# Kernel tuning notes

Hardware: AMD Instinct MI355X
Metric: run time of the kernel (lower is better)

## Reference

```python
import jax, jax.numpy as jnp
import numpy as np

VOCAB, EMBED, ENC_DIM, HIDDEN, ATTN = 32000, 512, 512, 1024, 128
SRC_LEN, TGT_LEN = 1024, 512


def setup_inputs() -> dict:
    key = jax.random.key(0)
    ks = jax.random.split(key, 16)
    s = lambda fan_in: 1.0 / np.sqrt(fan_in)
    inp = {
        "encoder_outputs": jax.random.normal(ks[0], (SRC_LEN, ENC_DIM), jnp.float32),
        "initial_h": jax.random.normal(ks[1], (HIDDEN,), jnp.float32),
        "initial_c": jnp.zeros((HIDDEN,), jnp.float32),
        "sos_token": 1,
        "target_seq": jax.random.randint(ks[2], (TGT_LEN,), 0, VOCAB, jnp.int32),
        # parameters
        "emb_table": jax.random.normal(ks[3], (VOCAB, EMBED), jnp.float32),
        "Wa_enc": jax.random.normal(ks[4], (ATTN, ENC_DIM), jnp.float32) * s(ENC_DIM),
        "Wa_h": jax.random.normal(ks[5], (ATTN, HIDDEN), jnp.float32) * s(HIDDEN),
        "v_a": jax.random.normal(ks[6], (ATTN,), jnp.float32) * s(ATTN),
        "W_ih": jax.random.normal(ks[7], (4 * HIDDEN, EMBED + ENC_DIM), jnp.float32) * s(EMBED + ENC_DIM),
        "W_hh": jax.random.normal(ks[8], (4 * HIDDEN, HIDDEN), jnp.float32) * s(HIDDEN),
        "b_ih": jnp.zeros((4 * HIDDEN,), jnp.float32),
        "b_hh": jnp.zeros((4 * HIDDEN,), jnp.float32),
        "W_out": jax.random.normal(ks[9], (VOCAB, HIDDEN), jnp.float32) * s(HIDDEN),
        "b_out": jnp.zeros((VOCAB,), jnp.float32),
    }
    return inp


def reference(encoder_outputs, initial_h, initial_c, sos_token, target_seq,
              emb_table, Wa_enc, Wa_h, v_a, W_ih, W_hh, b_ih, b_hh, W_out, b_out):
    # Teacher forcing with ratio 1.0: input token at step t is target_seq[t-1] (sos at t=0).
    prev_tokens = jnp.concatenate([jnp.array([sos_token], dtype=target_seq.dtype), target_seq[:-1]])
    embedded = emb_table[prev_tokens]                      # (T, E)
    enc_proj = encoder_outputs @ Wa_enc.T                  # (S, A), precomputed once

    def step(carry, emb_t):
        h, c = carry
        # Bahdanau attention: v^T tanh(W_enc e_s + W_h h)
        scores = jnp.tanh(enc_proj + Wa_h @ h) @ v_a       # (S,)
        attn = jax.nn.softmax(scores)                      # (S,)
        context = attn @ encoder_outputs                   # (ENC_DIM,)
        x = jnp.concatenate([emb_t, context])              # (E + ENC_DIM,)
        gates = W_ih @ x + b_ih + W_hh @ h + b_hh          # (4H,) order i,f,g,o
        i, f, g, o = jnp.split(gates, 4)
        c_new = jax.nn.sigmoid(f) * c + jax.nn.sigmoid(i) * jnp.tanh(g)
        h_new = jax.nn.sigmoid(o) * jnp.tanh(c_new)
        logits = W_out @ h_new + b_out                     # (V,)
        return (h_new, c_new), (logits, attn)

    (_, _), (all_logits, all_attn) = jax.lax.scan(step, (initial_h, initial_c), embedded)
    return all_logits, all_attn                            # (T, V), (T, S)
```

## Files before the change

### kernel.cpp

```cpp
#include <hip/hip_runtime.h>
#include <hip/hip_bf16.h>

#define VOCAB 32000
#define EMBED 512
#define ENCD  512
#define HID   1024
#define ATTN  128
#define SRC   1024
#define TGT   512
#define NB    64
#define NT    512
#define CHUNK 16

typedef __hip_bfloat16 bf16;
typedef _Float16 f16;
typedef __attribute__((ext_vector_type(2))) _Float16 f16x2;
typedef __attribute__((ext_vector_type(8))) _Float16 f16x8;
typedef __attribute__((ext_vector_type(8))) short bf16x8v;
typedef __attribute__((ext_vector_type(4))) float f32x4;

#define OFF_TP    0
#define OFF_G     131072
#define OFF_HH    1179648
#define OFF_CC    1704960
#define OFF_WAHG  1705984
#define OFF_PB    1706240
#define OFF_HBUF  1708288
#define OFF_CTR   1709312
#define OFF_WAHW  1709376
#define OFF_WHH   1774912
#define OFF_VT    3872064

__device__ __forceinline__ float sigm(float x){ return 1.f/(1.f+__expf(-x)); }
__device__ __forceinline__ float tanh_f(float x){
  float ax = fabsf(x);
  float e = __expf(-2.f*ax);
  float r = (1.f - e) / (1.f + e);
  return copysignf(r, x);
}
__device__ __forceinline__ short f2bs(float x){
  union { bf16 h; short s; } u; u.h = __float2bfloat16(x); return u.s;
}
__device__ __forceinline__ bf16x8v cvt8(const float* p){
  float4 a = *reinterpret_cast<const float4*>(p);
  float4 b = *reinterpret_cast<const float4*>(p+4);
  bf16x8v r;
  r[0]=f2bs(a.x); r[1]=f2bs(a.y); r[2]=f2bs(a.z); r[3]=f2bs(a.w);
  r[4]=f2bs(b.x); r[5]=f2bs(b.y); r[6]=f2bs(b.z); r[7]=f2bs(b.w);
  return r;
}
__device__ __forceinline__ float aldf(const float* p){
  return __hip_atomic_load(p, __ATOMIC_RELAXED, __HIP_MEMORY_SCOPE_AGENT);
}
__device__ __forceinline__ void astf(float* p, float v){
  __hip_atomic_store(p, v, __ATOMIC_RELAXED, __HIP_MEMORY_SCOPE_AGENT);
}
__device__ __forceinline__ unsigned aldu(const unsigned* p){
  return __hip_atomic_load(p, __ATOMIC_RELAXED, __HIP_MEMORY_SCOPE_AGENT);
}
__device__ __forceinline__ void astu(unsigned* p, unsigned v){
  __hip_atomic_store(p, v, __ATOMIC_RELAXED, __HIP_MEMORY_SCOPE_AGENT);
}

__global__ void k_encTP(const float* __restrict__ enc, const float* __restrict__ Wa_enc,
                        const float* __restrict__ v_a, unsigned* __restrict__ TP){
  __shared__ float eL[16][ENCD];
  int s0 = blockIdx.x*16, tid = threadIdx.x;
  #pragma unroll
  for (int i=0;i<16;i++){
    int li = tid + i*128;
    int t = li>>7, k4 = li&127;
    *reinterpret_cast<float4*>(&eL[t][k4*4]) =
      *reinterpret_cast<const float4*>(enc + (size_t)(s0+t)*ENCD + k4*4);
  }
  __syncthreads();
  const float* w = Wa_enc + (size_t)tid*ENCD;
  float va = v_a[tid];
  float acc[16];
  #pragma unroll
  for (int t=0;t<16;t++) acc[t]=0.f;
  for (int k4=0;k4<128;k4++){
    float4 wv = *reinterpret_cast<const float4*>(w + k4*4);
    #pragma unroll
    for (int t=0;t<16;t++){
      float4 e4 = *reinterpret_cast<const float4*>(&eL[t][k4*4]);
      acc[t] += wv.x*e4.x + wv.y*e4.y + wv.z*e4.z + wv.w*e4.w;
    }
  }
  #pragma unroll
  for (int t=0;t<16;t++){
    float th = tanh_f(acc[t]);
    th = fminf(0.9995f, fmaxf(-0.9995f, th));
    union { f16x2 h; unsigned u; } cv;
    cv.h = (f16x2){ (f16)th, (f16)(va*th) };
    TP[(size_t)(s0+t)*ATTN + tid] = cv.u;
  }
}

__global__ void k_gbase(const int* __restrict__ sos, const int* __restrict__ tgt,
                        const float* __restrict__ embt, const float* __restrict__ W_ih,
                        const float* __restrict__ b_ih, const float* __restrict__ b_hh,
                        f16* __restrict__ Gp){
  __shared__ float eL[16][EMBED];
  int tid = threadIdx.x;
  int t0 = blockIdx.y*16;
  #pragma unroll
  for (int i=0;i<8;i++){
    int li = tid + i*256;
    int t = li>>7, k4 = li&127;
    int tg = t0 + t;
    int tok = (tg==0) ? sos[0] : tgt[tg-1];
    *reinterpret_cast<float4*>(&eL[t][k4*4]) =
      *reinterpret_cast<const float4*>(embt + (size_t)tok*EMBED + k4*4);
  }
  __syncthreads();
  int r = blockIdx.x*256 + tid;
  int g = r>>10, j = r&1023;
  int prow = (j>>4)*64 + g*16 + (j&15);
  const float* w = W_ih + (size_t)r*(EMBED+ENCD);
  float base = b_ih[r] + b_hh[r];
  float acc[16];
  #pragma unroll
  for (int t=0;t<16;t++) acc[t]=0.f;
  for (int k4=0;k4<128;k4++){
    float4 wv = *reinterpret_cast<const float4*>(w + k4*4);
    #pragma unroll
    for (int t=0;t<16;t++){
      float4 e4 = *reinterpret_cast<const float4*>(&eL[t][k4*4]);
      acc[t] += wv.x*e4.x + wv.y*e4.y + wv.z*e4.z + wv.w*e4.w;
    }
  }
  #pragma unroll
  for (int t=0;t<16;t++) Gp[(size_t)(t0+t)*4096 + prow] = (f16)(acc[t] + base);
}

__global__ void k_cvt_whh(const float* __restrict__ W, f16* __restrict__ out){
  int r = blockIdx.x;
  int g = r >> 10, j = r & 1023;
  int prow = (j>>4)*64 + g*16 + (j&15);
  int k0 = threadIdx.x*8;
  float4 a = *reinterpret_cast<const float4*>(W + (size_t)r*HID + k0);
  float4 c = *reinterpret_cast<const float4*>(W + (size_t)r*HID + k0 + 4);
  f16x8 v = { (f16)a.x,(f16)a.y,(f16)a.z,(f16)a.w,(f16)c.x,(f16)c.y,(f16)c.z,(f16)c.w };
  *reinterpret_cast<f16x8*>(out + (size_t)prow*HID + k0) = v;
}
__global__ void k_cvt_wah(const float* __restrict__ W, f16* __restrict__ out){
  int r = blockIdx.x;
  int k0 = threadIdx.x*8;
  float4 a = *reinterpret_cast<const float4*>(W + (size_t)r*HID + k0);
  float4 c = *reinterpret_cast<const float4*>(W + (size_t)r*HID + k0 + 4);
  f16x8 v = { (f16)a.x,(f16)a.y,(f16)a.z,(f16)a.w,(f16)c.x,(f16)c.y,(f16)c.z,(f16)c.w };
  *reinterpret_cast<f16x8*>(out + (size_t)r*HID + k0) = v;
}

__global__ __launch_bounds__(256) void k_gemmV(const float* __restrict__ W_ih,
                                               const float* __restrict__ enc,
                                               f16* __restrict__ Vt){
  int bn = blockIdx.x, bm = blockIdx.y;
  int tid = threadIdx.x;
  int wid = tid>>6, lane = tid&63;
  int wr = wid>>1, wc = wid&1;
  int rowf = lane&15, kg = lane>>4;
  const int m_base = bm*128 + wr*64;
  const int n_base = bn*128 + wc*64;
  const float* Ap[4];
  #pragma unroll
  for (int mt=0;mt<4;mt++){
    int prow = m_base + mt*16 + rowf;
    int bb = prow>>6, g = (prow>>4)&3, jl = prow&15;
    int r = g*HID + bb*16 + jl;
    Ap[mt] = W_ih + (size_t)r*(EMBED+ENCD) + EMBED + kg*8;
  }
  const float* Bp = enc + (size_t)(n_base + rowf)*ENCD + kg*8;
  f32x4 acc[4][4];
  #pragma unroll
  for (int i=0;i<4;i++)
    #pragma unroll
    for (int jv=0;jv<4;jv++) acc[i][jv] = (f32x4){0.f,0.f,0.f,0.f};
  for (int kk=0; kk<ENCD; kk+=32){
    bf16x8v av[4], bv[4];
    #pragma unroll
    for (int mt=0;mt<4;mt++) av[mt] = cvt8(Ap[mt] + kk);
    #pragma unroll
    for (int nt=0;nt<4;nt++) bv[nt] = cvt8(Bp + (size_t)nt*16*ENCD + kk);
    #pragma unroll
    for (int mt=0;mt<4;mt++)
      #pragma unroll
      for (int nt=0;nt<4;nt++)
        acc[mt][nt] = __builtin_amdgcn_mfma_f32_16x16x32_bf16(av[mt], bv[nt], acc[mt][nt], 0,0,0);
  }
  #pragma unroll
  for (int mt=0;mt<4;mt++){
    #pragma unroll
    for (int nt=0;nt<4;nt++){
      int n = n_base + nt*16 + rowf;
      #pragma unroll
      for (int i=0;i<4;i++){
        int m = m_base + mt*16 + kg*4 + i;
        Vt[(size_t)m*SRC + n] = (f16)acc[mt][nt][i];
      }
    }
  }
}

__global__ void k_prep0(const float* __restrict__ h0, const float* __restrict__ c0,
                        float* __restrict__ Hh, float* __restrict__ Cc,
                        unsigned* __restrict__ hbuf, unsigned* __restrict__ ctr){
  int b = blockIdx.x, tid = threadIdx.x;
  int i = b*128 + tid;
  Hh[i] = h0[i];
  Cc[i] = c0[i];
  if (i < 512){
    union { f16x2 h; unsigned u; } cv;
    cv.h = (f16x2){ (f16)h0[2*i], (f16)h0[2*i+1] };
    hbuf[i] = cv.u;
  }
  if (i < 3) ctr[i] = 0u;
}

__global__ __launch_bounds__(NT) void k_multi(int t0,
    const unsigned* __restrict__ TP, const f16* __restrict__ Wah_h,
    const f16* __restrict__ Whh_h, const f16* __restrict__ Vt,
    const f16* __restrict__ Gp, const float* __restrict__ v_a,
    float* __restrict__ Hh, float* __restrict__ Cc,
    float* __restrict__ wahg, float* __restrict__ pbuf,
    unsigned* __restrict__ hbuf, unsigned* __restrict__ ctr,
    float* __restrict__ Pout)
{
  const int b = blockIdx.x, tid = threadIdx.x;
  __shared__ f16x8 hs8[128];
  __shared__ f16x8 ps8[128];
  __shared__ float2 vwp[128];
  __shared__ float vas[128];
  __shared__ float gacc[64];
  __shared__ float g2[64];
  __shared__ float pown[16];
  __shared__ float hnl[16];
  __shared__ float wpart[8];
  __shared__ float invs;
  __shared__ float cst[16];

  const int l8 = tid >> 3, q8 = tid & 7;

  if (tid < 16) cst[tid] = Cc[b*16 + tid];
  if (tid < 128) vas[tid] = v_a[tid];

  for (int k = 0; k < CHUNK; ++k){
    const int t = t0 + k;
    const unsigned base = 64u*(unsigned)t;
    if (tid == 0){
      while (aldu(&ctr[2]) < base) __builtin_amdgcn_s_sleep(1);
    }
    __syncthreads();
    if (tid < 128){
      const unsigned* hp = hbuf + (t&1)*512 + tid*4;
      union { unsigned u[4]; f16x8 v; } cv;
      cv.u[0]=aldu(hp); cv.u[1]=aldu(hp+1); cv.u[2]=aldu(hp+2); cv.u[3]=aldu(hp+3);
      hs8[(tid&15)*8 + (tid>>4)] = cv.v;
    }
    __syncthreads();
    if (tid < 128){
      int w = tid >> 6, lane = tid & 63;
      const f16x8* wr = (const f16x8*)(Wah_h + (size_t)(2*b+w)*HID) + lane;
      float acc = 0.f;
      #pragma unroll
      for (int i = 0; i < 2; ++i){
        int m = lane + i*64;
        f16x8 wv = wr[i*64];
        f16x8 hv = hs8[(m&15)*8 + (m>>4)];
        const f16x2* wp = (const f16x2*)&wv;
        const f16x2* hp = (const f16x2*)&hv;
        acc = __builtin_amdgcn_fdot2(wp[0], hp[0], acc, false);
        acc = __builtin_amdgcn_fdot2(wp[1], hp[1], acc, false);
        acc = __builtin_amdgcn_fdot2(wp[2], hp[2], acc, false);
        acc = __builtin_amdgcn_fdot2(wp[3], hp[3], acc, false);
      }
      acc += __shfl_xor(acc,1); acc += __shfl_xor(acc,2); acc += __shfl_xor(acc,4);
      acc += __shfl_xor(acc,8); acc += __shfl_xor(acc,16); acc += __shfl_xor(acc,32);
      if (lane == 0) astf(&wahg[(t&1)*128 + 2*b + w], acc);
    }
    __syncthreads();
    if (tid == 0)
      __hip_atomic_fetch_add(&ctr[0], 1u, __ATOMIC_RELAXED, __HIP_MEMORY_SCOPE_AGENT);
    {
      const f16x8* wr = (const f16x8*)(Whh_h + (size_t)(b*64 + l8)*HID + q8*128);
      float acc = 0.f;
      #pragma unroll
      for (int i = 0; i < 16; ++i){
        f16x8 wv = wr[i];
        f16x8 hv = hs8[i*8 + q8];
        const f16x2* wp = (const f16x2*)&wv;
        const f16x2* hp = (const f16x2*)&hv;
        acc = __builtin_amdgcn_fdot2(wp[0], hp[0], acc, false);
        acc = __builtin_amdgcn_fdot2(wp[1], hp[1], acc, false);
        acc = __builtin_amdgcn_fdot2(wp[2], hp[2], acc, false);
        acc = __builtin_amdgcn_fdot2(wp[3], hp[3], acc, false);
      }
      acc += __shfl_xor(acc,1); acc += __shfl_xor(acc,2); acc += __shfl_xor(acc,4);
      if (q8 == 0) gacc[l8] = acc;
    }
    if (tid == 0){
      while (aldu(&ctr[0]) < base + 64u) __builtin_amdgcn_s_sleep(1);
    }
    __syncthreads();
    if (tid < 128){
      float w = aldf(&wahg[(t&1)*128 + tid]);
      float tw = tanh_f(w);
      vwp[tid] = make_float2(tw, vas[tid]*tw);
    }
    __syncthreads();
    {
      int row = tid >> 5, l5 = tid & 31;
      const f16x8* tp8 = (const f16x8*)((const f16*)TP + ((size_t)(b*16+row)*ATTN + l5*4)*2);
      f16x8 tv = tp8[0];
      float sc = 0.f;
      #pragma unroll
      for (int u = 0; u < 4; ++u){
        float T  = (float)tv[2*u];
        float vT = (float)tv[2*u+1];
        float2 vw = vwp[l5*4 + u];
        float num = vT + vw.y;
        float den = fmaf(T, vw.x, 1.f);
        sc = fmaf(num, __builtin_amdgcn_rcpf(den), sc);
      }
      sc += __shfl_xor(sc,1); sc += __shfl_xor(sc,2); sc += __shfl_xor(sc,4);
      sc += __shfl_xor(sc,8); sc += __shfl_xor(sc,16);
      if (l5 == 0){
        float pv = __expf(sc);
        pown[row] = pv;
        astf(&pbuf[(t&1)*1024 + b*16 + row], pv);
      }
    }
    __syncthreads();
    if (tid == 0)
      __hip_atomic_fetch_add(&ctr[1], 1u, __ATOMIC_RELAXED, __HIP_MEMORY_SCOPE_AGENT);
    if (tid == 0){
      while (aldu(&ctr[1]) < base + 64u) __builtin_amdgcn_s_sleep(1);
    }
    __syncthreads();
    {
      float p0 = aldf(&pbuf[(t&1)*1024 + 2*tid]);
      float p1 = aldf(&pbuf[(t&1)*1024 + 2*tid + 1]);
      float s2 = p0 + p1;
      s2 += __shfl_xor(s2,1); s2 += __shfl_xor(s2,2); s2 += __shfl_xor(s2,4);
      s2 += __shfl_xor(s2,8); s2 += __shfl_xor(s2,16); s2 += __shfl_xor(s2,32);
      if ((tid & 63) == 0) wpart[tid >> 6] = s2;
      __syncthreads();
      if (tid == 0){
        float d = 0.f;
        #pragma unroll
        for (int kk = 0; kk < 8; ++kk) d += wpart[kk];
        invs = 1.f/d;
      }
      __syncthreads();
      float iv = invs;
      int q = tid >> 6, i8 = (tid & 63) >> 2, j = tid & 3;
      ((f16x2*)&ps8[i8*8 + q])[j] = (f16x2){ (f16)(p0*iv), (f16)(p1*iv) };
      if (tid < 16) Pout[(size_t)t*SRC + b*16 + tid] = pown[tid]*iv;
    }
    __syncthreads();
    {
      const f16x8* wr = (const f16x8*)(Vt + (size_t)(b*64 + l8)*SRC + q8*128);
      float acc = 0.f;
      #pragma unroll
      for (int i = 0; i < 16; ++i){
        f16x8 wv = wr[i];
        f16x8 pv = ps8[i*8 + q8];
        const f16x2* wp = (const f16x2*)&wv;
        const f16x2* pp = (const f16x2*)&pv;
        acc = __builtin_amdgcn_fdot2(wp[0], pp[0], acc, false);
        acc = __builtin_amdgcn_fdot2(wp[1], pp[1], acc, false);
        acc = __builtin_amdgcn_fdot2(wp[2], pp[2], acc, false);
        acc = __builtin_amdgcn_fdot2(wp[3], pp[3], acc, false);
      }
      acc += __shfl_xor(acc,1); acc += __shfl_xor(acc,2); acc += __shfl_xor(acc,4);
      if (q8 == 0) g2[l8] = acc + gacc[l8] + (float)Gp[(size_t)t*4096 + b*64 + l8];
    }
    __syncthreads();
    if (tid < 16){
      float gi = g2[tid], gf = g2[16+tid], gg = g2[32+tid], go = g2[48+tid];
      float cn = sigm(gf)*cst[tid] + sigm(gi)*tanh_f(gg);
      float hn = sigm(go)*tanh_f(cn);
      cst[tid] = cn;
      hnl[tid] = hn;
      Hh[(size_t)(t+1)*HID + b*16 + tid] = hn;
    }
    __syncthreads();
    if (tid < 8){
      union { f16x2 h; unsigned u; } cv;
      cv.h = (f16x2){ (f16)hnl[2*tid], (f16)hnl[2*tid+1] };
      astu(&hbuf[((t+1)&1)*512 + b*8 + tid], cv.u);
    }
    __syncthreads();
    if (tid == 0)
      __hip_atomic_fetch_add(&ctr[2], 1u, __ATOMIC_RELAXED, __HIP_MEMORY_SCOPE_AGENT);
  }
  if (tid < 16) Cc[b*16 + tid] = cst[tid];
}

__global__ __launch_bounds__(256) void k_gemm(const float* __restrict__ A, const float* __restrict__ B,
                                              const float* __restrict__ bias, float* __restrict__ C){
  int bn = blockIdx.x, bm = blockIdx.y;
  int tid = threadIdx.x;
  int wid = tid>>6, lane = tid&63;
  int wr = wid>>1, wc = wid&1;
  int rowf = lane&15, kg = lane>>4;
  const int m_base = bm*128 + wr*64;
  const int n_base = bn*128 + wc*64;
  const float* Ap = A + (size_t)(m_base + rowf)*HID + kg*8;
  const float* Bp = B + (size_t)(n_base + rowf)*HID + kg*8;
  f32x4 acc[4][4];
  #pragma unroll
  for (int i=0;i<4;i++)
    #pragma unroll
    for (int jv=0;jv<4;jv++) acc[i][jv] = (f32x4){0.f,0.f,0.f,0.f};
  for (int kk=0; kk<HID; kk+=32){
    bf16x8v av[4], bv[4];
    #pragma unroll
    for (int mt=0;mt<4;mt++) av[mt] = cvt8(Ap + (size_t)mt*16*HID + kk);
    #pragma unroll
    for (int nt=0;nt<4;nt++) bv[nt] = cvt8(Bp + (size_t)nt*16*HID + kk);
    #pragma unroll
    for (int mt=0;mt<4;mt++)
      #pragma unroll
      for (int nt=0;nt<4;nt++)
        acc[mt][nt] = __builtin_amdgcn_mfma_f32_16x16x32_bf16(av[mt], bv[nt], acc[mt][nt], 0,0,0);
  }
  #pragma unroll
  for (int mt=0;mt<4;mt++){
    #pragma unroll
    for (int nt=0;nt<4;nt++){
      int n = n_base + nt*16 + rowf;
      float bo = bias[n];
      #pragma unroll
      for (int i=0;i<4;i++){
        int m = m_base + mt*16 + kg*4 + i;
        C[(size_t)m*VOCAB + n] = acc[mt][nt][i] + bo;
      }
    }
  }
}

extern "C" void kernel_launch(void* const* d_in, const int* in_sizes, int n_in,
                              void* d_out, int out_size, void* d_ws, size_t ws_size,
                              hipStream_t stream){
  const float* enc    = (const float*)d_in[0];
  const float* h0     = (const float*)d_in[1];
  const float* c0     = (const float*)d_in[2];
  const int*   sos    = (const int*)d_in[3];
  const int*   tgt    = (const int*)d_in[4];
  const float* embt   = (const float*)d_in[5];
  const float* Wa_enc = (const float*)d_in[6];
  const float* Wa_h   = (const float*)d_in[7];
  const float* v_a    = (const float*)d_in[8];
  const float* W_ih   = (const float*)d_in[9];
  const float* W_hh   = (const float*)d_in[10];
  const float* b_ih   = (const float*)d_in[11];
  const float* b_hh   = (const float*)d_in[12];
  const float* W_out  = (const float*)d_in[13];
  const float* b_out  = (const float*)d_in[14];

  float* ws   = (float*)d_ws;
  unsigned* TP = (unsigned*)(ws + OFF_TP);
  f16*   Gp   = (f16*)(ws + OFF_G);
  float* Hh   = ws + OFF_HH;
  float* Cc   = ws + OFF_CC;
  float* wahg = ws + OFF_WAHG;
  float* pbuf = ws + OFF_PB;
  unsigned* hbuf = (unsigned*)(ws + OFF_HBUF);
  unsigned* ctr  = (unsigned*)(ws + OFF_CTR);
  f16*   Wah_h= (f16*)(ws + OFF_WAHW);
  f16*   Whh_h= (f16*)(ws + OFF_WHH);
  f16*   Vt   = (f16*)(ws + OFF_VT);

  float* out_logits = (float*)d_out;
  float* out_attn   = out_logits + (size_t)TGT*VOCAB;

  k_encTP   <<<64, 128, 0, stream>>>(enc, Wa_enc, v_a, TP);
  k_gbase   <<<dim3(16, 32), 256, 0, stream>>>(sos, tgt, embt, W_ih, b_ih, b_hh, Gp);
  k_cvt_whh <<<4096, 128, 0, stream>>>(W_hh, Whh_h);
  k_cvt_wah <<<128, 128, 0, stream>>>(Wa_h, Wah_h);
  k_gemmV   <<<dim3(8, 32), 256, 0, stream>>>(W_ih, enc, Vt);
  k_prep0   <<<8, 128, 0, stream>>>(h0, c0, Hh, Cc, hbuf, ctr);

  for (int t0 = 0; t0 < TGT; t0 += CHUNK){
    k_multi<<<NB, NT, 0, stream>>>(t0, TP, Wah_h, Whh_h, Vt, Gp, v_a,
                                   Hh, Cc, wahg, pbuf, hbuf, ctr, out_attn);
  }

  k_gemm<<<dim3(250, 4), 256, 0, stream>>>(Hh + HID, W_out, b_out, out_logits);
}
```

Before: 4.217 ms.

## Replace global counters with per-block flag slots and double the recurrent block count

Replaces the three shared atomic counters in the persistent recurrent kernel with per-block flag arrays that each block sets and all blocks poll in parallel. This removes fetch-add contention and single-thread polling. The recurrence now uses 128 blocks of 256 threads, each owning 8 hidden units, and the weight permutations are re-laid out to match. The W_hh matvec is split around the barriers so it overlaps the waits, fewer kernel launches are issued (chunk 64), and the output GEMM grid is remapped for locality. In exchange, every block polls 128 flags per barrier, and the gains rely on all 128 blocks being co-resident.

```diff
diff --git a/kernel.cpp b/kernel.cpp
--- a/kernel.cpp
+++ b/kernel.cpp
@@ -8,9 +8,9 @@
 #define ATTN  128
 #define SRC   1024
 #define TGT   512
-#define NB    64
-#define NT    512
-#define CHUNK 16
+#define NB    128
+#define NT    256
+#define CHUNK 64
 
 typedef __hip_bfloat16 bf16;
 typedef _Float16 f16;
@@ -26,10 +26,10 @@
 #define OFF_WAHG  1705984
 #define OFF_PB    1706240
 #define OFF_HBUF  1708288
-#define OFF_CTR   1709312
-#define OFF_WAHW  1709376
-#define OFF_WHH   1774912
-#define OFF_VT    3872064
+#define OFF_SLOT  1709312
+#define OFF_WAHW  1709824
+#define OFF_WHH   1775360
+#define OFF_VT    3872512
 
 __device__ __forceinline__ float sigm(float x){ return 1.f/(1.f+__expf(-x)); }
 __device__ __forceinline__ float tanh_f(float x){
@@ -61,6 +61,12 @@
 __device__ __forceinline__ void astu(unsigned* p, unsigned v){
   __hip_atomic_store(p, v, __ATOMIC_RELAXED, __HIP_MEMORY_SCOPE_AGENT);
 }
+__device__ __forceinline__ void waitslot(const unsigned* sl, unsigned tgt, int tid){
+  if (tid < NB){
+    while (aldu(&sl[tid]) < tgt) __builtin_amdgcn_s_sleep(1);
+  }
+  __syncthreads();
+}
 
 __global__ void k_encTP(const float* __restrict__ enc, const float* __restrict__ Wa_enc,
                         const float* __restrict__ v_a, unsigned* __restrict__ TP){
@@ -116,7 +122,7 @@
   __syncthreads();
   int r = blockIdx.x*256 + tid;
   int g = r>>10, j = r&1023;
-  int prow = (j>>4)*64 + g*16 + (j&15);
+  int prow = (j>>3)*32 + g*8 + (j&7);
   const float* w = W_ih + (size_t)r*(EMBED+ENCD);
   float base = b_ih[r] + b_hh[r];
   float acc[16];
@@ -137,7 +143,7 @@
 __global__ void k_cvt_whh(const float* __restrict__ W, f16* __restrict__ out){
   int r = blockIdx.x;
   int g = r >> 10, j = r & 1023;
-  int prow = (j>>4)*64 + g*16 + (j&15);
+  int prow = (j>>3)*32 + g*8 + (j&7);
   int k0 = threadIdx.x*8;
   float4 a = *reinterpret_cast<const float4*>(W + (size_t)r*HID + k0);
   float4 c = *reinterpret_cast<const float4*>(W + (size_t)r*HID + k0 + 4);
@@ -167,8 +173,8 @@
   #pragma unroll
   for (int mt=0;mt<4;mt++){
     int prow = m_base + mt*16 + rowf;
-    int bb = prow>>6, g = (prow>>4)&3, jl = prow&15;
-    int r = g*HID + bb*16 + jl;
+    int bb = prow>>5, g = (prow>>3)&3, jl = prow&7;
+    int r = g*HID + bb*8 + jl;
     Ap[mt] = W_ih + (size_t)r*(EMBED+ENCD) + EMBED + kg*8;
   }
   const float* Bp = enc + (size_t)(n_base + rowf)*ENCD + kg*8;
@@ -205,7 +211,7 @@
 
 __global__ void k_prep0(const float* __restrict__ h0, const float* __restrict__ c0,
                         float* __restrict__ Hh, float* __restrict__ Cc,
-                        unsigned* __restrict__ hbuf, unsigned* __restrict__ ctr){
+                        unsigned* __restrict__ hbuf, unsigned* __restrict__ slot){
   int b = blockIdx.x, tid = threadIdx.x;
   int i = b*128 + tid;
   Hh[i] = h0[i];
@@ -215,7 +221,11 @@
     cv.h = (f16x2){ (f16)h0[2*i], (f16)h0[2*i+1] };
     hbuf[i] = cv.u;
   }
-  if (i < 3) ctr[i] = 0u;
+  if (b == 0 && tid < NB){
+    slot[tid]         = 1u;
+    slot[NB + tid]    = 0u;
+    slot[2*NB + tid]  = 0u;
+  }
 }
 
 __global__ __launch_bounds__(NT) void k_multi(int t0,
@@ -224,34 +234,35 @@
     const f16* __restrict__ Gp, const float* __restrict__ v_a,
     float* __restrict__ Hh, float* __restrict__ Cc,
     float* __restrict__ wahg, float* __restrict__ pbuf,
-    unsigned* __restrict__ hbuf, unsigned* __restrict__ ctr,
+    unsigned* __restrict__ hbuf, unsigned* __restrict__ slot,
     float* __restrict__ Pout)
 {
   const int b = blockIdx.x, tid = threadIdx.x;
+  unsigned* slh = (unsigned*)slot;
+  unsigned* slw = (unsigned*)slot + NB;
+  unsigned* slp = (unsigned*)slot + 2*NB;
   __shared__ f16x8 hs8[128];
   __shared__ f16x8 ps8[128];
   __shared__ float2 vwp[128];
   __shared__ float vas[128];
-  __shared__ float gacc[64];
-  __shared__ float g2[64];
-  __shared__ float pown[16];
-  __shared__ float hnl[16];
-  __shared__ float wpart[8];
+  __shared__ float w2[2];
+  __shared__ float gacc[32];
+  __shared__ float g2[32];
+  __shared__ float pown[8];
+  __shared__ float hnl[8];
+  __shared__ float wpart[4];
   __shared__ float invs;
-  __shared__ float cst[16];
+  __shared__ float cst[8];
 
   const int l8 = tid >> 3, q8 = tid & 7;
 
-  if (tid < 16) cst[tid] = Cc[b*16 + tid];
+  if (tid < 8)   cst[tid] = Cc[b*8 + tid];
   if (tid < 128) vas[tid] = v_a[tid];
 
   for (int k = 0; k < CHUNK; ++k){
     const int t = t0 + k;
-    const unsigned base = 64u*(unsigned)t;
-    if (tid == 0){
-      while (aldu(&ctr[2]) < base) __builtin_amdgcn_s_sleep(1);
-    }
-    __syncthreads();
+    const unsigned tg1 = (unsigned)(t + 1);
+    waitslot(slh, tg1, tid);
     if (tid < 128){
       const unsigned* hp = hbuf + (t&1)*512 + tid*4;
       union { unsigned u[4]; f16x8 v; } cv;
@@ -260,49 +271,41 @@
     }
     __syncthreads();
     if (tid < 128){
-      int w = tid >> 6, lane = tid & 63;
-      const f16x8* wr = (const f16x8*)(Wah_h + (size_t)(2*b+w)*HID) + lane;
+      f16x8 wv = ((const f16x8*)(Wah_h + (size_t)b*HID))[tid];
+      f16x8 hv = hs8[(tid&15)*8 + (tid>>4)];
+      const f16x2* wp = (const f16x2*)&wv;
+      const f16x2* hp = (const f16x2*)&hv;
       float acc = 0.f;
-      #pragma unroll
-      for (int i = 0; i < 2; ++i){
-        int m = lane + i*64;
-        f16x8 wv = wr[i*64];
-        f16x8 hv = hs8[(m&15)*8 + (m>>4)];
-        const f16x2* wp = (const f16x2*)&wv;
-        const f16x2* hp = (const f16x2*)&hv;
-        acc = __builtin_amdgcn_fdot2(wp[0], hp[0], acc, false);
-        acc = __builtin_amdgcn_fdot2(wp[1], hp[1], acc, false);
-        acc = __builtin_amdgcn_fdot2(wp[2], hp[2], acc, false);
-        acc = __builtin_amdgcn_fdot2(wp[3], hp[3], acc, false);
-      }
+      acc = __builtin_amdgcn_fdot2(wp[0], hp[0], acc, false);
+      acc = __builtin_amdgcn_fdot2(wp[1], hp[1], acc, false);
+      acc = __builtin_amdgcn_fdot2(wp[2], hp[2], acc, false);
+      acc = __builtin_amdgcn_fdot2(wp[3], hp[3], acc, false);
       acc += __shfl_xor(acc,1); acc += __shfl_xor(acc,2); acc += __shfl_xor(acc,4);
       acc += __shfl_xor(acc,8); acc += __shfl_xor(acc,16); acc += __shfl_xor(acc,32);
-      if (lane == 0) astf(&wahg[(t&1)*128 + 2*b + w], acc);
-    }
-    __syncthreads();
-    if (tid == 0)
-      __hip_atomic_fetch_add(&ctr[0], 1u, __ATOMIC_RELAXED, __HIP_MEMORY_SCOPE_AGENT);
+      if ((tid & 63) == 0) w2[tid>>6] = acc;
+    }
+    __syncthreads();
+    if (tid == 0){
+      astf(&wahg[(t&1)*128 + b], w2[0] + w2[1]);
+      asm volatile("s_waitcnt vmcnt(0)");
+      astu(&slw[b], tg1);
+    }
+    float ga = 0.f;
     {
-      const f16x8* wr = (const f16x8*)(Whh_h + (size_t)(b*64 + l8)*HID + q8*128);
-      float acc = 0.f;
-      #pragma unroll
-      for (int i = 0; i < 16; ++i){
+      const f16x8* wr = (const f16x8*)(Whh_h + (size_t)(b*32 + l8)*HID + q8*128);
+      #pragma unroll
+      for (int i = 0; i < 8; ++i){
         f16x8 wv = wr[i];
         f16x8 hv = hs8[i*8 + q8];
         const f16x2* wp = (const f16x2*)&wv;
         const f16x2* hp = (const f16x2*)&hv;
-        acc = __builtin_amdgcn_fdot2(wp[0], hp[0], acc, false);
-        acc = __builtin_amdgcn_fdot2(wp[1], hp[1], acc, false);
-        acc = __builtin_amdgcn_fdot2(wp[2], hp[2], acc, false);
-        acc = __builtin_amdgcn_fdot2(wp[3], hp[3], acc, false);
-      }
-      acc += __shfl_xor(acc,1); acc += __shfl_xor(acc,2); acc += __shfl_xor(acc,4);
-      if (q8 == 0) gacc[l8] = acc;
-    }
-    if (tid == 0){
-      while (aldu(&ctr[0]) < base + 64u) __builtin_amdgcn_s_sleep(1);
-    }
-    __syncthreads();
+        ga = __builtin_amdgcn_fdot2(wp[0], hp[0], ga, false);
+        ga = __builtin_amdgcn_fdot2(wp[1], hp[1], ga, false);
+        ga = __builtin_amdgcn_fdot2(wp[2], hp[2], ga, false);
+        ga = __builtin_amdgcn_fdot2(wp[3], hp[3], ga, false);
+      }
+    }
+    waitslot(slw, tg1, tid);
     if (tid < 128){
       float w = aldf(&wahg[(t&1)*128 + tid]);
       float tw = tanh_f(w);
@@ -311,7 +314,7 @@
     __syncthreads();
     {
       int row = tid >> 5, l5 = tid & 31;
-      const f16x8* tp8 = (const f16x8*)((const f16*)TP + ((size_t)(b*16+row)*ATTN + l5*4)*2);
+      const f16x8* tp8 = (const f16x8*)((const f16*)TP + ((size_t)(b*8+row)*ATTN + l5*4)*2);
       f16x8 tv = tp8[0];
       float sc = 0.f;
       #pragma unroll
@@ -328,39 +331,48 @@
       if (l5 == 0){
         float pv = __expf(sc);
         pown[row] = pv;
-        astf(&pbuf[(t&1)*1024 + b*16 + row], pv);
-      }
-    }
-    __syncthreads();
-    if (tid == 0)
-      __hip_atomic_fetch_add(&ctr[1], 1u, __ATOMIC_RELAXED, __HIP_MEMORY_SCOPE_AGENT);
-    if (tid == 0){
-      while (aldu(&ctr[1]) < base + 64u) __builtin_amdgcn_s_sleep(1);
-    }
-    __syncthreads();
+        astf(&pbuf[(t&1)*1024 + b*8 + row], pv);
+      }
+    }
+    __syncthreads();
+    if (tid == 0) astu(&slp[b], tg1);
     {
-      float p0 = aldf(&pbuf[(t&1)*1024 + 2*tid]);
-      float p1 = aldf(&pbuf[(t&1)*1024 + 2*tid + 1]);
-      float s2 = p0 + p1;
-      s2 += __shfl_xor(s2,1); s2 += __shfl_xor(s2,2); s2 += __shfl_xor(s2,4);
-      s2 += __shfl_xor(s2,8); s2 += __shfl_xor(s2,16); s2 += __shfl_xor(s2,32);
-      if ((tid & 63) == 0) wpart[tid >> 6] = s2;
+      const f16x8* wr = (const f16x8*)(Whh_h + (size_t)(b*32 + l8)*HID + q8*128);
+      #pragma unroll
+      for (int i = 8; i < 16; ++i){
+        f16x8 wv = wr[i];
+        f16x8 hv = hs8[i*8 + q8];
+        const f16x2* wp = (const f16x2*)&wv;
+        const f16x2* hp = (const f16x2*)&hv;
+        ga = __builtin_amdgcn_fdot2(wp[0], hp[0], ga, false);
+        ga = __builtin_amdgcn_fdot2(wp[1], hp[1], ga, false);
+        ga = __builtin_amdgcn_fdot2(wp[2], hp[2], ga, false);
+        ga = __builtin_amdgcn_fdot2(wp[3], hp[3], ga, false);
+      }
+      ga += __shfl_xor(ga,1); ga += __shfl_xor(ga,2); ga += __shfl_xor(ga,4);
+      if (q8 == 0) gacc[l8] = ga;
+    }
+    waitslot(slp, tg1, tid);
+    {
+      const float* pb = pbuf + (t&1)*1024 + tid*4;
+      float p0 = aldf(pb), p1 = aldf(pb+1), p2 = aldf(pb+2), p3 = aldf(pb+3);
+      float s4 = (p0+p1) + (p2+p3);
+      s4 += __shfl_xor(s4,1); s4 += __shfl_xor(s4,2); s4 += __shfl_xor(s4,4);
+      s4 += __shfl_xor(s4,8); s4 += __shfl_xor(s4,16); s4 += __shfl_xor(s4,32);
+      if ((tid & 63) == 0) wpart[tid>>6] = s4;
       __syncthreads();
-      if (tid == 0){
-        float d = 0.f;
-        #pragma unroll
-        for (int kk = 0; kk < 8; ++kk) d += wpart[kk];
-        invs = 1.f/d;
-      }
+      if (tid == 0) invs = 1.f/((wpart[0]+wpart[1]) + (wpart[2]+wpart[3]));
       __syncthreads();
       float iv = invs;
-      int q = tid >> 6, i8 = (tid & 63) >> 2, j = tid & 3;
-      ((f16x2*)&ps8[i8*8 + q])[j] = (f16x2){ (f16)(p0*iv), (f16)(p1*iv) };
-      if (tid < 16) Pout[(size_t)t*SRC + b*16 + tid] = pown[tid]*iv;
+      int c = tid >> 1, half = tid & 1;
+      f16x2* dst = (f16x2*)&ps8[(c&15)*8 + (c>>4)];
+      dst[2*half]   = (f16x2){ (f16)(p0*iv), (f16)(p1*iv) };
+      dst[2*half+1] = (f16x2){ (f16)(p2*iv), (f16)(p3*iv) };
+      if (tid < 8) Pout[(size_t)t*SRC + b*8 + tid] = pown[tid]*iv;
     }
     __syncthreads();
     {
-      const f16x8* wr = (const f16x8*)(Vt + (size_t)(b*64 + l8)*SRC + q8*128);
+      const f16x8* wr = (const f16x8*)(Vt + (size_t)(b*32 + l8)*SRC + q8*128);
       float acc = 0.f;
       #pragma unroll
       for (int i = 0; i < 16; ++i){
@@ -374,33 +386,34 @@
         acc = __builtin_amdgcn_fdot2(wp[3], pp[3], acc, false);
       }
       acc += __shfl_xor(acc,1); acc += __shfl_xor(acc,2); acc += __shfl_xor(acc,4);
-      if (q8 == 0) g2[l8] = acc + gacc[l8] + (float)Gp[(size_t)t*4096 + b*64 + l8];
-    }
-    __syncthreads();
-    if (tid < 16){
-      float gi = g2[tid], gf = g2[16+tid], gg = g2[32+tid], go = g2[48+tid];
+      if (q8 == 0) g2[l8] = acc + gacc[l8] + (float)Gp[(size_t)t*4096 + b*32 + l8];
+    }
+    __syncthreads();
+    if (tid < 8){
+      float gi = g2[tid], gf = g2[8+tid], gg = g2[16+tid], go = g2[24+tid];
       float cn = sigm(gf)*cst[tid] + sigm(gi)*tanh_f(gg);
       float hn = sigm(go)*tanh_f(cn);
       cst[tid] = cn;
       hnl[tid] = hn;
-      Hh[(size_t)(t+1)*HID + b*16 + tid] = hn;
-    }
-    __syncthreads();
-    if (tid < 8){
+      Hh[(size_t)(t+1)*HID + b*8 + tid] = hn;
+    }
+    __syncthreads();
+    if (tid < 4){
       union { f16x2 h; unsigned u; } cv;
       cv.h = (f16x2){ (f16)hnl[2*tid], (f16)hnl[2*tid+1] };
-      astu(&hbuf[((t+1)&1)*512 + b*8 + tid], cv.u);
-    }
-    __syncthreads();
-    if (tid == 0)
-      __hip_atomic_fetch_add(&ctr[2], 1u, __ATOMIC_RELAXED, __HIP_MEMORY_SCOPE_AGENT);
-  }
-  if (tid < 16) Cc[b*16 + tid] = cst[tid];
+      astu(&hbuf[((t+1)&1)*512 + b*4 + tid], cv.u);
+    }
+    __syncthreads();
+    if (tid == 0) astu(&slh[b], tg1 + 1u);
+  }
+  if (tid < 8) Cc[b*8 + tid] = cst[tid];
 }
 
 __global__ __launch_bounds__(256) void k_gemm(const float* __restrict__ A, const float* __restrict__ B,
                                               const float* __restrict__ bias, float* __restrict__ C){
-  int bn = blockIdx.x, bm = blockIdx.y;
+  int bid = blockIdx.x;
+  int tile = (bid & 7)*125 + (bid >> 3);
+  int bm = tile & 3, bn = tile >> 2;
   int tid = threadIdx.x;
   int wid = tid>>6, lane = tid&63;
   int wr = wid>>1, wc = wid&1;
@@ -468,7 +481,7 @@
   float* wahg = ws + OFF_WAHG;
   float* pbuf = ws + OFF_PB;
   unsigned* hbuf = (unsigned*)(ws + OFF_HBUF);
-  unsigned* ctr  = (unsigned*)(ws + OFF_CTR);
+  unsigned* slot = (unsigned*)(ws + OFF_SLOT);
   f16*   Wah_h= (f16*)(ws + OFF_WAHW);
   f16*   Whh_h= (f16*)(ws + OFF_WHH);
   f16*   Vt   = (f16*)(ws + OFF_VT);
@@ -481,12 +494,12 @@
   k_cvt_whh <<<4096, 128, 0, stream>>>(W_hh, Whh_h);
   k_cvt_wah <<<128, 128, 0, stream>>>(Wa_h, Wah_h);
   k_gemmV   <<<dim3(8, 32), 256, 0, stream>>>(W_ih, enc, Vt);
-  k_prep0   <<<8, 128, 0, stream>>>(h0, c0, Hh, Cc, hbuf, ctr);
+  k_prep0   <<<8, 128, 0, stream>>>(h0, c0, Hh, Cc, hbuf, slot);
 
   for (int t0 = 0; t0 < TGT; t0 += CHUNK){
     k_multi<<<NB, NT, 0, stream>>>(t0, TP, Wah_h, Whh_h, Vt, Gp, v_a,
-                                   Hh, Cc, wahg, pbuf, hbuf, ctr, out_attn);
-  }
-
-  k_gemm<<<dim3(250, 4), 256, 0, stream>>>(Hh + HID, W_out, b_out, out_logits);
-}
+                                   Hh, Cc, wahg, pbuf, hbuf, slot, out_attn);
+  }
+
+  k_gemm<<<1000, 256, 0, stream>>>(Hh + HID, W_out, b_out, out_logits);
+}
```

After: 7.115 ms. 1.69x slower.

## Fold Wa_h·h into previous step to drop a grid barrier per timestep

Applied to the files above, without the earlier changes.

Each block now computes partial Wa_h products for its own 16 new hidden units at the end of step t and publishes them. The next step sums the 16 partials directly, so the separate wahg phase and its grid-wide counter wait go away. The W_hh matvec moves after the attention barrier so it overlaps the wait. The chunk size grows to 64 steps, cutting the number of persistent-kernel relaunches, and the output GEMM gets a swizzled 1D tile order. The cost is extra global partial-sum traffic (16 loads per attention row per step) and a transposed Wa_h layout.

```diff
diff --git a/kernel.cpp b/kernel.cpp
--- a/kernel.cpp
+++ b/kernel.cpp
@@ -10,7 +10,7 @@
 #define TGT   512
 #define NB    64
 #define NT    512
-#define CHUNK 16
+#define CHUNK 64
 
 typedef __hip_bfloat16 bf16;
 typedef _Float16 f16;
@@ -23,13 +23,13 @@
 #define OFF_G     131072
 #define OFF_HH    1179648
 #define OFF_CC    1704960
-#define OFF_WAHG  1705984
-#define OFF_PB    1706240
-#define OFF_HBUF  1708288
-#define OFF_CTR   1709312
-#define OFF_WAHW  1709376
-#define OFF_WHH   1774912
-#define OFF_VT    3872064
+#define OFF_WAHPB 1705984
+#define OFF_PB    1722368
+#define OFF_HBUF  1724416
+#define OFF_CTR   1725440
+#define OFF_WAHT  1725504
+#define OFF_WHH   1791040
+#define OFF_VT    3888192
 
 __device__ __forceinline__ float sigm(float x){ return 1.f/(1.f+__expf(-x)); }
 __device__ __forceinline__ float tanh_f(float x){
@@ -144,13 +144,18 @@
   f16x8 v = { (f16)a.x,(f16)a.y,(f16)a.z,(f16)a.w,(f16)c.x,(f16)c.y,(f16)c.z,(f16)c.w };
   *reinterpret_cast<f16x8*>(out + (size_t)prow*HID + k0) = v;
 }
-__global__ void k_cvt_wah(const float* __restrict__ W, f16* __restrict__ out){
-  int r = blockIdx.x;
-  int k0 = threadIdx.x*8;
-  float4 a = *reinterpret_cast<const float4*>(W + (size_t)r*HID + k0);
-  float4 c = *reinterpret_cast<const float4*>(W + (size_t)r*HID + k0 + 4);
-  f16x8 v = { (f16)a.x,(f16)a.y,(f16)a.z,(f16)a.w,(f16)c.x,(f16)c.y,(f16)c.z,(f16)c.w };
-  *reinterpret_cast<f16x8*>(out + (size_t)r*HID + k0) = v;
+__global__ void k_cvt_wahT(const float* __restrict__ W, f16* __restrict__ out){
+  int b = blockIdx.x, a = threadIdx.x;
+  const float* src = W + (size_t)a*HID + b*16;
+  float4 v0 = *reinterpret_cast<const float4*>(src);
+  float4 v1 = *reinterpret_cast<const float4*>(src+4);
+  float4 v2 = *reinterpret_cast<const float4*>(src+8);
+  float4 v3 = *reinterpret_cast<const float4*>(src+12);
+  f16* dst = out + ((size_t)b*128 + a)*16;
+  f16x8 w0 = { (f16)v0.x,(f16)v0.y,(f16)v0.z,(f16)v0.w,(f16)v1.x,(f16)v1.y,(f16)v1.z,(f16)v1.w };
+  f16x8 w1 = { (f16)v2.x,(f16)v2.y,(f16)v2.z,(f16)v2.w,(f16)v3.x,(f16)v3.y,(f16)v3.z,(f16)v3.w };
+  *reinterpret_cast<f16x8*>(dst)   = w0;
+  *reinterpret_cast<f16x8*>(dst+8) = w1;
 }
 
 __global__ __launch_bounds__(256) void k_gemmV(const float* __restrict__ W_ih,
@@ -204,26 +209,38 @@
 }
 
 __global__ void k_prep0(const float* __restrict__ h0, const float* __restrict__ c0,
+                        const float* __restrict__ Wa_h,
                         float* __restrict__ Hh, float* __restrict__ Cc,
-                        unsigned* __restrict__ hbuf, unsigned* __restrict__ ctr){
+                        unsigned* __restrict__ hbuf, float* __restrict__ wahpb,
+                        unsigned* __restrict__ ctr){
   int b = blockIdx.x, tid = threadIdx.x;
-  int i = b*128 + tid;
-  Hh[i] = h0[i];
-  Cc[i] = c0[i];
-  if (i < 512){
+  if (b < 8){ Hh[b*128+tid] = h0[b*128+tid]; Cc[b*128+tid] = c0[b*128+tid]; }
+  if (b < 4){
+    int i = b*128 + tid;
     union { f16x2 h; unsigned u; } cv;
     cv.h = (f16x2){ (f16)h0[2*i], (f16)h0[2*i+1] };
     hbuf[i] = cv.u;
   }
-  if (i < 3) ctr[i] = 0u;
+  if (b == 0 && tid < 3) ctr[tid] = 0u;
+  __shared__ float hl[16];
+  if (tid < 16) hl[tid] = h0[b*16 + tid];
+  __syncthreads();
+  const float* wr = Wa_h + (size_t)tid*HID + b*16;
+  float acc = 0.f;
+  #pragma unroll
+  for (int i4=0;i4<4;i4++){
+    float4 w4 = *reinterpret_cast<const float4*>(wr + i4*4);
+    acc += w4.x*hl[i4*4] + w4.y*hl[i4*4+1] + w4.z*hl[i4*4+2] + w4.w*hl[i4*4+3];
+  }
+  wahpb[b*128 + tid] = acc;
 }
 
 __global__ __launch_bounds__(NT) void k_multi(int t0,
-    const unsigned* __restrict__ TP, const f16* __restrict__ Wah_h,
+    const unsigned* __restrict__ TP, const f16* __restrict__ WahT,
     const f16* __restrict__ Whh_h, const f16* __restrict__ Vt,
     const f16* __restrict__ Gp, const float* __restrict__ v_a,
     float* __restrict__ Hh, float* __restrict__ Cc,
-    float* __restrict__ wahg, float* __restrict__ pbuf,
+    float* __restrict__ wahpb, float* __restrict__ pbuf,
     unsigned* __restrict__ hbuf, unsigned* __restrict__ ctr,
     float* __restrict__ Pout)
 {
@@ -236,13 +253,14 @@
   __shared__ float g2[64];
   __shared__ float pown[16];
   __shared__ float hnl[16];
+  __shared__ f16x2 hnl2[8];
   __shared__ float wpart[8];
   __shared__ float invs;
   __shared__ float cst[16];
 
   const int l8 = tid >> 3, q8 = tid & 7;
 
-  if (tid < 16) cst[tid] = Cc[b*16 + tid];
+  if (tid < 16)  cst[tid] = Cc[b*16 + tid];
   if (tid < 128) vas[tid] = v_a[tid];
 
   for (int k = 0; k < CHUNK; ++k){
@@ -258,55 +276,17 @@
       cv.u[0]=aldu(hp); cv.u[1]=aldu(hp+1); cv.u[2]=aldu(hp+2); cv.u[3]=aldu(hp+3);
       hs8[(tid&15)*8 + (tid>>4)] = cv.v;
     }
-    __syncthreads();
-    if (tid < 128){
-      int w = tid >> 6, lane = tid & 63;
-      const f16x8* wr = (const f16x8*)(Wah_h + (size_t)(2*b+w)*HID) + lane;
+    {
+      int a = tid >> 2, lane4 = tid & 3;
+      const float* wp = wahpb + (t&1)*8192 + lane4*128 + a;
       float acc = 0.f;
       #pragma unroll
-      for (int i = 0; i < 2; ++i){
-        int m = lane + i*64;
-        f16x8 wv = wr[i*64];
-        f16x8 hv = hs8[(m&15)*8 + (m>>4)];
-        const f16x2* wp = (const f16x2*)&wv;
-        const f16x2* hp = (const f16x2*)&hv;
-        acc = __builtin_amdgcn_fdot2(wp[0], hp[0], acc, false);
-        acc = __builtin_amdgcn_fdot2(wp[1], hp[1], acc, false);
-        acc = __builtin_amdgcn_fdot2(wp[2], hp[2], acc, false);
-        acc = __builtin_amdgcn_fdot2(wp[3], hp[3], acc, false);
-      }
-      acc += __shfl_xor(acc,1); acc += __shfl_xor(acc,2); acc += __shfl_xor(acc,4);
-      acc += __shfl_xor(acc,8); acc += __shfl_xor(acc,16); acc += __shfl_xor(acc,32);
-      if (lane == 0) astf(&wahg[(t&1)*128 + 2*b + w], acc);
-    }
-    __syncthreads();
-    if (tid == 0)
-      __hip_atomic_fetch_add(&ctr[0], 1u, __ATOMIC_RELAXED, __HIP_MEMORY_SCOPE_AGENT);
-    {
-      const f16x8* wr = (const f16x8*)(Whh_h + (size_t)(b*64 + l8)*HID + q8*128);
-      float acc = 0.f;
-      #pragma unroll
-      for (int i = 0; i < 16; ++i){
-        f16x8 wv = wr[i];
-        f16x8 hv = hs8[i*8 + q8];
-        const f16x2* wp = (const f16x2*)&wv;
-        const f16x2* hp = (const f16x2*)&hv;
-        acc = __builtin_amdgcn_fdot2(wp[0], hp[0], acc, false);
-        acc = __builtin_amdgcn_fdot2(wp[1], hp[1], acc, false);
-        acc = __builtin_amdgcn_fdot2(wp[2], hp[2], acc, false);
-        acc = __builtin_amdgcn_fdot2(wp[3], hp[3], acc, false);
-      }
-      acc += __shfl_xor(acc,1); acc += __shfl_xor(acc,2); acc += __shfl_xor(acc,4);
-      if (q8 == 0) gacc[l8] = acc;
-    }
-    if (tid == 0){
-      while (aldu(&ctr[0]) < base + 64u) __builtin_amdgcn_s_sleep(1);
-    }
-    __syncthreads();
-    if (tid < 128){
-      float w = aldf(&wahg[(t&1)*128 + tid]);
-      float tw = tanh_f(w);
-      vwp[tid] = make_float2(tw, vas[tid]*tw);
+      for (int m = 0; m < 16; ++m) acc += aldf(wp + m*512);
+      acc += __shfl_xor(acc,1); acc += __shfl_xor(acc,2);
+      if (lane4 == 0){
+        float tw = tanh_f(acc);
+        vwp[a] = make_float2(tw, vas[a]*tw);
+      }
     }
     __syncthreads();
     {
@@ -334,6 +314,23 @@
     __syncthreads();
     if (tid == 0)
       __hip_atomic_fetch_add(&ctr[1], 1u, __ATOMIC_RELAXED, __HIP_MEMORY_SCOPE_AGENT);
+    {
+      const f16x8* wr = (const f16x8*)(Whh_h + (size_t)(b*64 + l8)*HID + q8*128);
+      float ga = 0.f;
+      #pragma unroll
+      for (int i = 0; i < 16; ++i){
+        f16x8 wv = wr[i];
+        f16x8 hv = hs8[i*8 + q8];
+        const f16x2* wp = (const f16x2*)&wv;
+        const f16x2* hp = (const f16x2*)&hv;
+        ga = __builtin_amdgcn_fdot2(wp[0], hp[0], ga, false);
+        ga = __builtin_amdgcn_fdot2(wp[1], hp[1], ga, false);
+        ga = __builtin_amdgcn_fdot2(wp[2], hp[2], ga, false);
+        ga = __builtin_amdgcn_fdot2(wp[3], hp[3], ga, false);
+      }
+      ga += __shfl_xor(ga,1); ga += __shfl_xor(ga,2); ga += __shfl_xor(ga,4);
+      if (q8 == 0) gacc[l8] = ga;
+    }
     if (tid == 0){
       while (aldu(&ctr[1]) < base + 64u) __builtin_amdgcn_s_sleep(1);
     }
@@ -386,10 +383,28 @@
       Hh[(size_t)(t+1)*HID + b*16 + tid] = hn;
     }
     __syncthreads();
+    if (tid < 8) hnl2[tid] = (f16x2){ (f16)hnl[2*tid], (f16)hnl[2*tid+1] };
+    __syncthreads();
     if (tid < 8){
       union { f16x2 h; unsigned u; } cv;
-      cv.h = (f16x2){ (f16)hnl[2*tid], (f16)hnl[2*tid+1] };
+      cv.h = hnl2[tid];
       astu(&hbuf[((t+1)&1)*512 + b*8 + tid], cv.u);
+    } else if (tid >= 128 && tid < 256){
+      int a = tid - 128;
+      const f16x8* wt = (const f16x8*)(WahT + ((size_t)b*128 + a)*16);
+      f16x8 w0 = wt[0], w1 = wt[1];
+      const f16x2* wp0 = (const f16x2*)&w0;
+      const f16x2* wp1 = (const f16x2*)&w1;
+      float acc = 0.f;
+      acc = __builtin_amdgcn_fdot2(wp0[0], hnl2[0], acc, false);
+      acc = __builtin_amdgcn_fdot2(wp0[1], hnl2[1], acc, false);
+      acc = __builtin_amdgcn_fdot2(wp0[2], hnl2[2], acc, false);
+      acc = __builtin_amdgcn_fdot2(wp0[3], hnl2[3], acc, false);
+      acc = __builtin_amdgcn_fdot2(wp1[0], hnl2[4], acc, false);
+      acc = __builtin_amdgcn_fdot2(wp1[1], hnl2[5], acc, false);
+      acc = __builtin_amdgcn_fdot2(wp1[2], hnl2[6], acc, false);
+      acc = __builtin_amdgcn_fdot2(wp1[3], hnl2[7], acc, false);
+      astf(&wahpb[((t+1)&1)*8192 + b*128 + a], acc);
     }
     __syncthreads();
     if (tid == 0)
@@ -400,7 +415,9 @@
 
 __global__ __launch_bounds__(256) void k_gemm(const float* __restrict__ A, const float* __restrict__ B,
                                               const float* __restrict__ bias, float* __restrict__ C){
-  int bn = blockIdx.x, bm = blockIdx.y;
+  int bid = blockIdx.x;
+  int tile = (bid & 7)*125 + (bid >> 3);
+  int bm = tile & 3, bn = tile >> 2;
   int tid = threadIdx.x;
   int wid = tid>>6, lane = tid&63;
   int wr = wid>>1, wc = wid&1;
@@ -465,11 +482,11 @@
   f16*   Gp   = (f16*)(ws + OFF_G);
   float* Hh   = ws + OFF_HH;
   float* Cc   = ws + OFF_CC;
-  float* wahg = ws + OFF_WAHG;
+  float* wahpb= ws + OFF_WAHPB;
   float* pbuf = ws + OFF_PB;
   unsigned* hbuf = (unsigned*)(ws + OFF_HBUF);
   unsigned* ctr  = (unsigned*)(ws + OFF_CTR);
-  f16*   Wah_h= (f16*)(ws + OFF_WAHW);
+  f16*   WahT = (f16*)(ws + OFF_WAHT);
   f16*   Whh_h= (f16*)(ws + OFF_WHH);
   f16*   Vt   = (f16*)(ws + OFF_VT);
 
@@ -479,14 +496,14 @@
   k_encTP   <<<64, 128, 0, stream>>>(enc, Wa_enc, v_a, TP);
   k_gbase   <<<dim3(16, 32), 256, 0, stream>>>(sos, tgt, embt, W_ih, b_ih, b_hh, Gp);
   k_cvt_whh <<<4096, 128, 0, stream>>>(W_hh, Whh_h);
-  k_cvt_wah <<<128, 128, 0, stream>>>(Wa_h, Wah_h);
+  k_cvt_wahT<<<64, 128, 0, stream>>>(Wa_h, WahT);
   k_gemmV   <<<dim3(8, 32), 256, 0, stream>>>(W_ih, enc, Vt);
-  k_prep0   <<<8, 128, 0, stream>>>(h0, c0, Hh, Cc, hbuf, ctr);
+  k_prep0   <<<64, 128, 0, stream>>>(h0, c0, Wa_h, Hh, Cc, hbuf, wahpb, ctr);
 
   for (int t0 = 0; t0 < TGT; t0 += CHUNK){
-    k_multi<<<NB, NT, 0, stream>>>(t0, TP, Wah_h, Whh_h, Vt, Gp, v_a,
-                                   Hh, Cc, wahg, pbuf, hbuf, ctr, out_attn);
-  }
-
-  k_gemm<<<dim3(250, 4), 256, 0, stream>>>(Hh + HID, W_out, b_out, out_logits);
-}
+    k_multi<<<NB, NT, 0, stream>>>(t0, TP, WahT, Whh_h, Vt, Gp, v_a,
+                                   Hh, Cc, wahpb, pbuf, hbuf, ctr, out_attn);
+  }
+
+  k_gemm<<<1000, 256, 0, stream>>>(Hh + HID, W_out, b_out, out_logits);
+}
```

Result: faster. 3.753 ms (-11.0%).
